# Optimization experiments

Hardware: AMD Instinct MI355X
Metric: run time of the kernel (lower is better)

Reference implementation:

```python
import jax, jax.numpy as jnp
import numpy as np

HEIGHT, WIDTH = 224, 224
SIGMA = 3e-4      # soft-coverage falloff (DIB-R style delta)
EPS = 1e-10


def setup_inputs() -> dict:
    key = jax.random.key(0)
    kp, kf, kc = jax.random.split(key, 3)
    B, P, F = 2, 2048, 256
    points = 0.5 * jax.random.normal(kp, (B, P, 3), dtype=jnp.float32)
    faces = jax.random.randint(kf, (F, 3), 0, P, dtype=jnp.int32)
    colors = jax.random.uniform(kc, (B, P, 3), dtype=jnp.float32)
    rot = jnp.broadcast_to(jnp.eye(3, dtype=jnp.float32), (B, 3, 3))
    pos = jnp.tile(jnp.array([0.0, 0.0, 2.5], jnp.float32), (B, 1))
    tanfov = float(np.tan(45.0 * np.pi / 360.0))
    proj = jnp.array([[1.0 / tanfov], [1.0 / tanfov], [-1.0]], jnp.float32)
    return dict(points_bxpx3=points, faces_fx3=faces, camera_rot=rot,
                camera_pos=pos, camera_proj=proj, colors_bxpx3=colors)


def _render(points_bxpx3, camera_rot, camera_pos, camera_proj, colors_bxpx3, faces_fx3):
    H, W = HEIGHT, WIDTH
    # ---- perspective projection (kaolin DIB-R convention) ----
    pc = jnp.einsum('bpj,bij->bpi', points_bxpx3 - camera_pos[:, None, :], camera_rot)  # camera space [B,P,3]
    xyz = pc * camera_proj.reshape(1, 1, 3)
    xy = xyz[..., :2] / xyz[..., 2:3]                                   # NDC xy [B,P,2]
    i0, i1, i2 = faces_fx3[:, 0], faces_fx3[:, 1], faces_fx3[:, 2]
    p0, p1, p2 = pc[:, i0], pc[:, i1], pc[:, i2]                        # [B,F,3]
    q0, q1, q2 = xy[:, i0], xy[:, i1], xy[:, i2]                        # [B,F,2]
    normal = jnp.cross(p1 - p0, p2 - p0)                                # [B,F,3]
    normalz = normal[..., 2]
    normal1 = normal / jnp.sqrt(jnp.sum(normal * normal, -1, keepdims=True) + EPS)
    # ---- per-face vertex features: 3 verts x (rgb + mask) == color_bxfx12 ----
    ones = jnp.ones(colors_bxpx3.shape[:2] + (1,), colors_bxpx3.dtype)
    cm = jnp.concatenate([colors_bxpx3, ones], -1)                      # [B,P,4]
    feat = jnp.stack([cm[:, i0], cm[:, i1], cm[:, i2]], axis=2)         # [B,F,3,4]
    # ---- rasterize: per-pixel per-face barycentric test ----
    xs = (2.0 * jnp.arange(W, dtype=jnp.float32) + 1.0) / W - 1.0
    ys = 1.0 - (2.0 * jnp.arange(H, dtype=jnp.float32) + 1.0) / H
    PX = xs[None, None, :, None]                                        # [1,1,W,1]
    PY = ys[None, :, None, None]                                        # [1,H,1,1]
    bf = lambda a: a[:, None, None, :]                                  # [B,F] -> [B,1,1,F]
    x0, y0 = q0[..., 0], q0[..., 1]
    x1, y1 = q1[..., 0], q1[..., 1]
    x2, y2 = q2[..., 0], q2[..., 1]
    denom = (y1 - y2) * (x0 - x2) + (x2 - x1) * (y0 - y2)
    denom = jnp.where(jnp.abs(denom) < EPS, EPS, denom)
    dx2 = PX - bf(x2)
    dy2 = PY - bf(y2)
    lam0 = (bf(y1 - y2) * dx2 + bf(x2 - x1) * dy2) / bf(denom)          # [B,H,W,F]
    lam1 = (bf(y2 - y0) * dx2 + bf(x0 - x2) * dy2) / bf(denom)
    lam2 = 1.0 - lam0 - lam1
    inside = (lam0 >= 0) & (lam1 >= 0) & (lam2 >= 0)
    front = (normalz > 0)[:, None, None, :]
    valid = inside & front
    # nearest face: camera looks down -z, nearer == larger camera-space z
    zpix = lam0 * bf(p0[..., 2]) + lam1 * bf(p1[..., 2]) + lam2 * bf(p2[..., 2])
    score = jnp.where(valid, zpix, -1e10)
    idx = jnp.argmax(score, axis=-1)                                    # [B,H,W]
    valid_any = jnp.any(valid, axis=-1)
    take = lambda a: jnp.take_along_axis(a, idx[..., None], axis=-1)[..., 0]
    l0, l1, l2 = take(lam0), take(lam1), take(lam2)
    fsel = jax.vmap(lambda f, i: f[i])(feat, idx)                       # [B,H,W,3,4]
    imfeat = (l0[..., None] * fsel[..., 0, :] + l1[..., None] * fsel[..., 1, :]
              + l2[..., None] * fsel[..., 2, :]) * valid_any[..., None]
    # ---- soft coverage probability: dist to nearest edge, 0 inside ----
    def seg_d2(ax, ay, bx, by):
        ex, ey = bf(bx - ax), bf(by - ay)
        pax, pay = PX - bf(ax), PY - bf(ay)
        t = jnp.clip((pax * ex + pay * ey) / (ex * ex + ey * ey + EPS), 0.0, 1.0)
        ddx, ddy = pax - t * ex, pay - t * ey
        return ddx * ddx + ddy * ddy
    d2 = jnp.minimum(seg_d2(x0, y0, x1, y1),
                     jnp.minimum(seg_d2(x1, y1, x2, y2), seg_d2(x2, y2, x0, y0)))
    d2 = jnp.where(inside, 0.0, d2)
    prob = jnp.where(front, jnp.exp(-d2 / SIGMA) * (1.0 - 1e-7), 0.0)
    improb = (1.0 - jnp.exp(jnp.sum(jnp.log1p(-prob), axis=-1)))[..., None]  # [B,H,W,1]
    imrender = imfeat[..., :3]
    return imrender, improb, normal1


def reference(points_bxpx3, camera_rot, camera_pos, camera_proj, colors_bxpx3, faces_fx3):
    return _render(points_bxpx3, camera_rot, camera_pos, camera_proj, colors_bxpx3, faces_fx3)
```

## Files before the change

kernel.cpp:

```cpp
#include <hip/hip_runtime.h>
#include <math.h>

#define HGT 224
#define WID 224
#define NPIX (HGT * WID)
#define SIGMA 0.0003f
#define EPSV 1e-10f
#define FILT_STRIDE 16
#define DATA_STRIDE 32
#define MARGIN 0.062f
#define HALFDIAG 0.04420f
#define BAND (MARGIN + HALFDIAG)


__global__ void face_pre(const float* __restrict__ points,
                         const int* __restrict__ faces,
                         const float* __restrict__ rot,
                         const float* __restrict__ pos,
                         const float* __restrict__ proj,
                         const float* __restrict__ colors,
                         float* __restrict__ filt,
                         float* __restrict__ data,
                         float* __restrict__ out_normal,
                         int B, int P, int F) {
    int gid = blockIdx.x * blockDim.x + threadIdx.x;
    if (gid >= B * F) return;
    int b = gid / F;
    int f = gid - b * F;

    const float* Rb = rot + b * 9;
    float posx = pos[b * 3 + 0], posy = pos[b * 3 + 1], posz = pos[b * 3 + 2];
    float pj0 = proj[0], pj1 = proj[1], pj2 = proj[2];

    float pcx[3], pcy[3], pcz[3], qx[3], qy[3], col[9];
    for (int v = 0; v < 3; v++) {
        int i = faces[f * 3 + v];
        float dx = points[(b * P + i) * 3 + 0] - posx;
        float dy = points[(b * P + i) * 3 + 1] - posy;
        float dz = points[(b * P + i) * 3 + 2] - posz;
        pcx[v] = Rb[0] * dx + Rb[1] * dy + Rb[2] * dz;
        pcy[v] = Rb[3] * dx + Rb[4] * dy + Rb[5] * dz;
        pcz[v] = Rb[6] * dx + Rb[7] * dy + Rb[8] * dz;
        float zz = pcz[v] * pj2;
        qx[v] = (pcx[v] * pj0) / zz;
        qy[v] = (pcy[v] * pj1) / zz;
        col[v * 3 + 0] = colors[(b * P + i) * 3 + 0];
        col[v * 3 + 1] = colors[(b * P + i) * 3 + 1];
        col[v * 3 + 2] = colors[(b * P + i) * 3 + 2];
    }

    float ux = pcx[1] - pcx[0], uy = pcy[1] - pcy[0], uz = pcz[1] - pcz[0];
    float vx = pcx[2] - pcx[0], vy = pcy[2] - pcy[0], vz = pcz[2] - pcz[0];
    float nx = uy * vz - uz * vy;
    float ny = uz * vx - ux * vz;
    float nz = ux * vy - uy * vx;
    float ninv = 1.0f / sqrtf(nx * nx + ny * ny + nz * nz + EPSV);
    out_normal[gid * 3 + 0] = nx * ninv;
    out_normal[gid * 3 + 1] = ny * ninv;
    out_normal[gid * 3 + 2] = nz * ninv;

    float x0 = qx[0], y0 = qy[0], x1 = qx[1], y1 = qy[1], x2 = qx[2], y2 = qy[2];
    float denom = (y1 - y2) * (x0 - x2) + (x2 - x1) * (y0 - y2);
    if (fabsf(denom) < EPSV) denom = EPSV;
    float rd = 1.0f / denom;

    float a00 = (y1 - y2) * rd;
    float a01 = (x2 - x1) * rd;
    float a10 = (y2 - y0) * rd;
    float a11 = (x0 - x2) * rd;

    float* fq = filt + gid * FILT_STRIDE;
    bool front = nz > 0.0f;
    fq[0] = front ? fminf(x0, fminf(x1, x2)) :  1e30f;
    fq[1] = front ? fminf(y0, fminf(y1, y2)) :  1e30f;
    fq[2] = front ? fmaxf(x0, fmaxf(x1, x2)) : -1e30f;
    fq[3] = front ? fmaxf(y0, fmaxf(y1, y2)) : -1e30f;

    float n0 = 1.0f / sqrtf(a00 * a00 + a01 * a01 + EPSV);
    float n1 = 1.0f / sqrtf(a10 * a10 + a11 * a11 + EPSV);
    float g2x = -(a00 + a10), g2y = -(a01 + a11);
    float n2 = 1.0f / sqrtf(g2x * g2x + g2y * g2y + EPSV);
    fq[4] = a00 * n0;
    fq[5] = a01 * n0;
    fq[6] = -(a00 * x2 + a01 * y2) * n0;
    fq[7] = a10 * n1;
    fq[8] = a11 * n1;
    fq[9] = -(a10 * x2 + a11 * y2) * n1;
    fq[10] = g2x * n2;
    fq[11] = g2y * n2;
    fq[12] = (1.0f - g2x * x2 - g2y * y2) * n2;
    fq[13] = 0.0f; fq[14] = 0.0f; fq[15] = 0.0f;

    float* fp = data + gid * DATA_STRIDE;
    fp[0] = x0; fp[1] = y0; fp[2] = x1; fp[3] = y1; fp[4] = x2; fp[5] = y2;
    fp[6] = a00; fp[7] = a01; fp[8] = a10; fp[9] = a11;
    fp[10] = pcz[0]; fp[11] = pcz[1]; fp[12] = pcz[2];
    fp[13] = 0.0f;
    for (int k = 0; k < 9; k++) fp[14 + k] = col[k];

    float e01x = x1 - x0, e01y = y1 - y0;
    float e12x = x2 - x1, e12y = y2 - y1;
    float e20x = x0 - x2, e20y = y0 - y2;
    fp[23] = e01x; fp[24] = e01y; fp[25] = 1.0f / (e01x * e01x + e01y * e01y + EPSV);
    fp[26] = e12x; fp[27] = e12y; fp[28] = 1.0f / (e12x * e12x + e12y * e12y + EPSV);
    fp[29] = e20x; fp[30] = e20y; fp[31] = 1.0f / (e20x * e20x + e20y * e20y + EPSV);
}

__device__ __forceinline__ float seg_d2(float px, float py, float ax, float ay,
                                        float ex, float ey, float inv) {
    float pax = px - ax, pay = py - ay;
    float t = (pax * ex + pay * ey) * inv;
    t = fminf(fmaxf(t, 0.0f), 1.0f);
    float ddx = pax - t * ex;
    float ddy = pay - t * ey;
    return ddx * ddx + ddy * ddy;
}

__global__ __launch_bounds__(256) void rast(const float* __restrict__ filt,
                                            const float* __restrict__ data,
                                            float* __restrict__ out,
                                            int B, int F) {
    const int tiles_x = WID / 8;
    const int tiles_per_batch = tiles_x * (HGT / 8);
    int b = blockIdx.x / tiles_per_batch;
    int tile = blockIdx.x - b * tiles_per_batch;
    int ty = tile / tiles_x;
    int tx = tile - ty * tiles_x;

    int t = threadIdx.x & 63;
    int w = threadIdx.x >> 6;
    int lx = t & 7, ly = t >> 3;
    int x = tx * 8 + lx;
    int y = ty * 8 + ly;
    float px = (2.0f * (float)x + 1.0f) / (float)WID - 1.0f;
    float py = 1.0f - (2.0f * (float)y + 1.0f) / (float)HGT;

    float txlo = (2.0f * (float)(tx * 8) + 1.0f) / (float)WID - 1.0f - MARGIN;
    float txhi = (2.0f * (float)(tx * 8 + 7) + 1.0f) / (float)WID - 1.0f + MARGIN;
    float tyhi = 1.0f - (2.0f * (float)(ty * 8) + 1.0f) / (float)HGT + MARGIN;
    float tylo = 1.0f - (2.0f * (float)(ty * 8 + 7) + 1.0f) / (float)HGT - MARGIN;
    float cx = (16.0f * (float)tx + 8.0f) / (float)WID - 1.0f;
    float cy = 1.0f - (16.0f * (float)ty + 8.0f) / (float)HGT;

    const float* fltb = filt + (size_t)b * F * FILT_STRIDE;
    const float* datb = data + (size_t)b * F * DATA_STRIDE;

    int chunk = (F + 3) >> 2;
    int fbeg = w * chunk;
    int fend = min(fbeg + chunk, F);

    float best = -1e10f;
    int bidx = -1;
    float bl0 = 0.0f, bl1 = 0.0f, bl2 = 0.0f;
    float prod = 1.0f;
    const float INSIDE_FACTOR = 1.0f - (1.0f - 1e-7f);

    for (int base = fbeg; base < fend; base += 64) {
        bool pass = false;
        int fl = base + t;
        if (fl < fend) {
            const float* fq = fltb + fl * FILT_STRIDE;
            float4 bb = *(const float4*)fq;
            float4 e0 = *(const float4*)(fq + 4);
            float4 e1 = *(const float4*)(fq + 8);
            float  dc2 = fq[12];
            bool bpass = (bb.x <= txhi) & (bb.z >= txlo) & (bb.y <= tyhi) & (bb.w >= tylo);
            float d0 = e0.x * cx + e0.y * cy + e0.z;
            float d1 = e0.w * cx + e1.x * cy + e1.y;
            float d2 = e1.z * cx + e1.w * cy + dc2;
            pass = bpass & (fminf(d0, fminf(d1, d2)) >= -BAND);
        }
        unsigned long long mask = __ballot(pass);

        while (mask) {
            int fo = (int)__builtin_ctzll(mask);
            mask &= mask - 1;
            int fi = base + fo;
            const float* fp = datb + fi * DATA_STRIDE;

            float dx2 = px - fp[4], dy2 = py - fp[5];
            float lam0 = fp[6] * dx2 + fp[7] * dy2;
            float lam1 = fp[8] * dx2 + fp[9] * dy2;
            float lam2 = 1.0f - lam0 - lam1;
            bool inside = (lam0 >= 0.0f) && (lam1 >= 0.0f) && (lam2 >= 0.0f);
            unsigned long long ins = __ballot(inside);

            if (ins) {
                float zpix = lam0 * fp[10] + lam1 * fp[11] + lam2 * fp[12];
                if (inside && zpix > best) {
                    best = zpix; bidx = fi;
                    bl0 = lam0; bl1 = lam1; bl2 = lam2;
                }
            }

            if (ins == ~0ULL) {
                prod *= INSIDE_FACTOR;
            } else {
                float dA = seg_d2(px, py, fp[0], fp[1], fp[23], fp[24], fp[25]);
                float dB = seg_d2(px, py, fp[2], fp[3], fp[26], fp[27], fp[28]);
                float dC = seg_d2(px, py, fp[4], fp[5], fp[29], fp[30], fp[31]);
                float d2 = inside ? 0.0f : fminf(dA, fminf(dB, dC));
                float pr = __expf(d2 * (-1.0f / SIGMA)) * (1.0f - 1e-7f);
                prod *= (1.0f - pr);
            }
        }
    }

    __shared__ float sc[256], sl0[256], sl1[256], sl2[256], sp[256];
    __shared__ int sidx[256];
    sc[threadIdx.x] = best;
    sl0[threadIdx.x] = bl0; sl1[threadIdx.x] = bl1; sl2[threadIdx.x] = bl2;
    sp[threadIdx.x] = prod;
    sidx[threadIdx.x] = bidx;
    __syncthreads();

    if (w == 0) {
        best = -1e10f; bidx = -1;
        bl0 = 0.0f; bl1 = 0.0f; bl2 = 0.0f;
        prod = 1.0f;
        for (int k = 0; k < 4; k++) {
            int j = k * 64 + t;
            prod *= sp[j];
            float v = sc[j];
            if (v > best) {
                best = v; bidx = sidx[j];
                bl0 = sl0[j]; bl1 = sl1[j]; bl2 = sl2[j];
            }
        }

        float r = 0.0f, g = 0.0f, bb = 0.0f;
        if (bidx >= 0) {
            const float* fp = datb + bidx * DATA_STRIDE;
            r  = bl0 * fp[14] + bl1 * fp[17] + bl2 * fp[20];
            g  = bl0 * fp[15] + bl1 * fp[18] + bl2 * fp[21];
            bb = bl0 * fp[16] + bl1 * fp[19] + bl2 * fp[22];
        }

        int pixidx = b * NPIX + y * WID + x;
        out[pixidx * 3 + 0] = r;
        out[pixidx * 3 + 1] = g;
        out[pixidx * 3 + 2] = bb;
        out[B * NPIX * 3 + pixidx] = 1.0f - prod;
    }
}

extern "C" void kernel_launch(void* const* d_in, const int* in_sizes, int n_in,
                              void* d_out, int out_size, void* d_ws, size_t ws_size,
                              hipStream_t stream) {
    const float* points = (const float*)d_in[0];
    const int*   faces  = (const int*)d_in[1];
    const float* rot    = (const float*)d_in[2];
    const float* pos    = (const float*)d_in[3];
    const float* proj   = (const float*)d_in[4];
    const float* colors = (const float*)d_in[5];
    float* out = (float*)d_out;

    int F = in_sizes[1] / 3;
    int B = in_sizes[3] / 3;
    int P = in_sizes[0] / (3 * B);

    float* filt = (float*)d_ws;
    float* data = filt + (size_t)B * F * FILT_STRIDE;
    float* out_normal = out + B * NPIX * 3 + B * NPIX;

    int nf = B * F;
    face_pre<<<(nf + 255) / 256, 256, 0, stream>>>(points, faces, rot, pos, proj,
                                                   colors, filt, data, out_normal,
                                                   B, P, F);

    int blocks = B * (NPIX / 64);
    rast<<<blocks, 256, 0, stream>>>(filt, data, out, B, F);
}
```

Before: 80.98 us.

## Split faces into fully-covering and boundary sets; defer barycentrics to final color

The per-tile filter now also classifies faces whose edge distances exceed the tile half-diagonal as fully covering the tile. Those faces take a fast path that evaluates depth with a precomputed plane gradient and applies the constant inside factor, skipping the barycentric inside test, the ballot and the edge-distance math. Barycentrics are no longer carried per thread or reduced through shared memory; they are recomputed once for the winning face when the color is written. The per-face data record is reordered so the hot fields sit first, and depth interpolation relies on a gradient form whose rounding may differ slightly from the original.

```diff
diff --git a/kernel.cpp b/kernel.cpp
--- a/kernel.cpp
+++ b/kernel.cpp
@@ -11,6 +11,7 @@
 #define MARGIN 0.062f
 #define HALFDIAG 0.04420f
 #define BAND (MARGIN + HALFDIAG)
+#define HD_IN (HALFDIAG + 1.0e-4f)
 
 
 __global__ void face_pre(const float* __restrict__ points,
@@ -91,19 +92,23 @@
     fq[12] = (1.0f - g2x * x2 - g2y * y2) * n2;
     fq[13] = 0.0f; fq[14] = 0.0f; fq[15] = 0.0f;
 
+    float z0 = pcz[0], z1 = pcz[1], z2c = pcz[2];
     float* fp = data + gid * DATA_STRIDE;
-    fp[0] = x0; fp[1] = y0; fp[2] = x1; fp[3] = y1; fp[4] = x2; fp[5] = y2;
-    fp[6] = a00; fp[7] = a01; fp[8] = a10; fp[9] = a11;
-    fp[10] = pcz[0]; fp[11] = pcz[1]; fp[12] = pcz[2];
-    fp[13] = 0.0f;
-    for (int k = 0; k < 9; k++) fp[14 + k] = col[k];
+    fp[0] = x2; fp[1] = y2;
+    fp[2] = a00 * (z0 - z2c) + a10 * (z1 - z2c);
+    fp[3] = a01 * (z0 - z2c) + a11 * (z1 - z2c);
+    fp[4] = z2c;
+    fp[5] = a00; fp[6] = a01; fp[7] = a10; fp[8] = a11;
+    fp[9] = x0; fp[10] = y0; fp[11] = x1; fp[12] = y1;
 
     float e01x = x1 - x0, e01y = y1 - y0;
     float e12x = x2 - x1, e12y = y2 - y1;
     float e20x = x0 - x2, e20y = y0 - y2;
-    fp[23] = e01x; fp[24] = e01y; fp[25] = 1.0f / (e01x * e01x + e01y * e01y + EPSV);
-    fp[26] = e12x; fp[27] = e12y; fp[28] = 1.0f / (e12x * e12x + e12y * e12y + EPSV);
-    fp[29] = e20x; fp[30] = e20y; fp[31] = 1.0f / (e20x * e20x + e20y * e20y + EPSV);
+    fp[13] = e01x; fp[14] = e01y; fp[15] = 1.0f / (e01x * e01x + e01y * e01y + EPSV);
+    fp[16] = e12x; fp[17] = e12y; fp[18] = 1.0f / (e12x * e12x + e12y * e12y + EPSV);
+    fp[19] = e20x; fp[20] = e20y; fp[21] = 1.0f / (e20x * e20x + e20y * e20y + EPSV);
+    for (int k = 0; k < 9; k++) fp[22 + k] = col[k];
+    fp[31] = 0.0f;
 }
 
 __device__ __forceinline__ float seg_d2(float px, float py, float ax, float ay,
@@ -151,12 +156,11 @@
 
     float best = -1e10f;
     int bidx = -1;
-    float bl0 = 0.0f, bl1 = 0.0f, bl2 = 0.0f;
     float prod = 1.0f;
     const float INSIDE_FACTOR = 1.0f - (1.0f - 1e-7f);
 
     for (int base = fbeg; base < fend; base += 64) {
-        bool pass = false;
+        bool pass = false, inclass = false;
         int fl = base + t;
         if (fl < fend) {
             const float* fq = fltb + fl * FILT_STRIDE;
@@ -168,55 +172,57 @@
             float d0 = e0.x * cx + e0.y * cy + e0.z;
             float d1 = e0.w * cx + e1.x * cy + e1.y;
             float d2 = e1.z * cx + e1.w * cy + dc2;
-            pass = bpass & (fminf(d0, fminf(d1, d2)) >= -BAND);
-        }
-        unsigned long long mask = __ballot(pass);
-
-        while (mask) {
-            int fo = (int)__builtin_ctzll(mask);
-            mask &= mask - 1;
+            float dmin = fminf(d0, fminf(d1, d2));
+            pass = bpass & (dmin >= -BAND);
+            inclass = bpass & (dmin >= HD_IN);
+        }
+        unsigned long long mask_in = __ballot(inclass);
+        unsigned long long mask_bd = __ballot(pass) & ~mask_in;
+
+        while (mask_in) {
+            int fo = (int)__builtin_ctzll(mask_in);
+            mask_in &= mask_in - 1;
             int fi = base + fo;
             const float* fp = datb + fi * DATA_STRIDE;
-
-            float dx2 = px - fp[4], dy2 = py - fp[5];
-            float lam0 = fp[6] * dx2 + fp[7] * dy2;
-            float lam1 = fp[8] * dx2 + fp[9] * dy2;
+            float dx2 = px - fp[0], dy2 = py - fp[1];
+            float zpix = fp[2] * dx2 + fp[3] * dy2 + fp[4];
+            if (zpix > best) { best = zpix; bidx = fi; }
+            prod *= INSIDE_FACTOR;
+        }
+
+        while (mask_bd) {
+            int fo = (int)__builtin_ctzll(mask_bd);
+            mask_bd &= mask_bd - 1;
+            int fi = base + fo;
+            const float* fp = datb + fi * DATA_STRIDE;
+
+            float dx2 = px - fp[0], dy2 = py - fp[1];
+            float lam0 = fp[5] * dx2 + fp[6] * dy2;
+            float lam1 = fp[7] * dx2 + fp[8] * dy2;
             float lam2 = 1.0f - lam0 - lam1;
             bool inside = (lam0 >= 0.0f) && (lam1 >= 0.0f) && (lam2 >= 0.0f);
-            unsigned long long ins = __ballot(inside);
-
-            if (ins) {
-                float zpix = lam0 * fp[10] + lam1 * fp[11] + lam2 * fp[12];
-                if (inside && zpix > best) {
-                    best = zpix; bidx = fi;
-                    bl0 = lam0; bl1 = lam1; bl2 = lam2;
-                }
-            }
-
-            if (ins == ~0ULL) {
-                prod *= INSIDE_FACTOR;
-            } else {
-                float dA = seg_d2(px, py, fp[0], fp[1], fp[23], fp[24], fp[25]);
-                float dB = seg_d2(px, py, fp[2], fp[3], fp[26], fp[27], fp[28]);
-                float dC = seg_d2(px, py, fp[4], fp[5], fp[29], fp[30], fp[31]);
-                float d2 = inside ? 0.0f : fminf(dA, fminf(dB, dC));
-                float pr = __expf(d2 * (-1.0f / SIGMA)) * (1.0f - 1e-7f);
-                prod *= (1.0f - pr);
-            }
+
+            float zpix = fp[2] * dx2 + fp[3] * dy2 + fp[4];
+            if (inside && zpix > best) { best = zpix; bidx = fi; }
+
+            float dA = seg_d2(px, py, fp[9],  fp[10], fp[13], fp[14], fp[15]);
+            float dB = seg_d2(px, py, fp[11], fp[12], fp[16], fp[17], fp[18]);
+            float dC = seg_d2(px, py, fp[0],  fp[1],  fp[19], fp[20], fp[21]);
+            float d2 = inside ? 0.0f : fminf(dA, fminf(dB, dC));
+            float pr = __expf(d2 * (-1.0f / SIGMA)) * (1.0f - 1e-7f);
+            prod *= (1.0f - pr);
         }
     }
 
-    __shared__ float sc[256], sl0[256], sl1[256], sl2[256], sp[256];
+    __shared__ float sc[256], sp[256];
     __shared__ int sidx[256];
     sc[threadIdx.x] = best;
-    sl0[threadIdx.x] = bl0; sl1[threadIdx.x] = bl1; sl2[threadIdx.x] = bl2;
     sp[threadIdx.x] = prod;
     sidx[threadIdx.x] = bidx;
     __syncthreads();
 
     if (w == 0) {
         best = -1e10f; bidx = -1;
-        bl0 = 0.0f; bl1 = 0.0f; bl2 = 0.0f;
         prod = 1.0f;
         for (int k = 0; k < 4; k++) {
             int j = k * 64 + t;
@@ -224,16 +230,19 @@
             float v = sc[j];
             if (v > best) {
                 best = v; bidx = sidx[j];
-                bl0 = sl0[j]; bl1 = sl1[j]; bl2 = sl2[j];
             }
         }
 
         float r = 0.0f, g = 0.0f, bb = 0.0f;
         if (bidx >= 0) {
             const float* fp = datb + bidx * DATA_STRIDE;
-            r  = bl0 * fp[14] + bl1 * fp[17] + bl2 * fp[20];
-            g  = bl0 * fp[15] + bl1 * fp[18] + bl2 * fp[21];
-            bb = bl0 * fp[16] + bl1 * fp[19] + bl2 * fp[22];
+            float dx2 = px - fp[0], dy2 = py - fp[1];
+            float lam0 = fp[5] * dx2 + fp[6] * dy2;
+            float lam1 = fp[7] * dx2 + fp[8] * dy2;
+            float lam2 = 1.0f - lam0 - lam1;
+            r  = lam0 * fp[22] + lam1 * fp[25] + lam2 * fp[28];
+            g  = lam0 * fp[23] + lam1 * fp[26] + lam2 * fp[29];
+            bb = lam0 * fp[24] + lam1 * fp[27] + lam2 * fp[30];
         }
 
         int pixidx = b * NPIX + y * WID + x;
```

After: 77.58 us. 4.2% less time.
